# Kernel tuning notes

Measured on AMD Instinct MI355X. Metric: run time of the kernel, lower is better.

The kernel has to match this reference:

```python
import jax, jax.numpy as jnp
import numpy as np
import math

LMAX = 5
TAU_PRE = 16
TAU = 16
B = 256


def _cg_coeff(l1, l2, l, m1, m2, m):
    # Standard Clebsch-Gordan coefficient <l1 m1 l2 m2 | l m> (Racah formula).
    if m1 + m2 != m or l < abs(l1 - l2) or l > l1 + l2:
        return 0.0
    f = math.factorial
    pref = math.sqrt((2 * l + 1) * f(l + l1 - l2) * f(l - l1 + l2) * f(l1 + l2 - l) / f(l1 + l2 + l + 1))
    pref *= math.sqrt(f(l + m) * f(l - m) * f(l1 - m1) * f(l1 + m1) * f(l2 - m2) * f(l2 + m2))
    kmin = max(0, l2 - l - m1, l1 + m2 - l)
    kmax = min(l1 + l2 - l, l1 - m1, l2 + m2)
    s = 0.0
    for k in range(kmin, kmax + 1):
        s += (-1) ** k / (f(k) * f(l1 + l2 - l - k) * f(l1 - m1 - k) * f(l2 + m2 - k) * f(l - l2 + m1 + k) * f(l - l1 - m2 + k))
    return pref * s


def _build_cg(lmax):
    # Enumerate (l1, l2<=l1, l) triples exactly as UpdateFunction._calculate_number_of_cols / fCG do.
    triples, tensors = [], {}
    for l1 in range(lmax + 1):
        for l2 in range(l1 + 1):
            for l in range(abs(l1 - l2), min(l1 + l2 + 1, lmax + 1)):
                C = np.zeros((2 * l + 1, 2 * l1 + 1, 2 * l2 + 1), dtype=np.float32)
                for m in range(-l, l + 1):
                    for m1 in range(-l1, l1 + 1):
                        m2 = m - m1
                        if -l2 <= m2 <= l2:
                            C[m + l, m1 + l1, m2 + l2] = _cg_coeff(l1, l2, l, m1, m2, m)
                triples.append((l1, l2, l))
                tensors[(l1, l2, l)] = jnp.asarray(C)
    return triples, tensors


TRIPLES, CG = _build_cg(LMAX)
NUMCOLS = [sum(TAU_PRE * TAU_PRE for (_, _, l) in TRIPLES if l == L) for L in range(LMAX + 1)]


def _cg_transform(fs):
    # CG tensor product: for each (l1,l2,l) triple form complex channel-pair products
    # contracted with CG coefficients; concat fragments along the channel axis per l.
    frags = [[] for _ in range(LMAX + 1)]
    for (l1, l2, l) in TRIPLES:
        C = CG[(l1, l2, l)]                       # [2l+1, 2l1+1, 2l2+1]
        f1, f2 = fs[l1], fs[l2]                   # [B, t, 2l*+1, 2]
        f1r, f1i = f1[..., 0], f1[..., 1]
        f2r, f2i = f2[..., 0], f2[..., 1]
        rr = jnp.einsum('kmn,bim,bjn->bijk', C, f1r, f2r)
        ii = jnp.einsum('kmn,bim,bjn->bijk', C, f1i, f2i)
        ri = jnp.einsum('kmn,bim,bjn->bijk', C, f1r, f2i)
        ir = jnp.einsum('kmn,bim,bjn->bijk', C, f1i, f2r)
        frag = jnp.stack([rr - ii, ri + ir], axis=-1)          # [B, t1, t2, 2l+1, 2]
        bsz = f1.shape[0]
        frags[l].append(frag.reshape(bsz, -1, 2 * l + 1, 2))
    return [jnp.concatenate(fl, axis=1) for fl in frags]       # per l: [B, numcols[l], 2l+1, 2]


def _complex_mm(w, f):
    # Complex_bmm with w broadcast over the batch: w [tau, cols, 2], f [B, cols, 2l+1, 2].
    wr, wi = w[..., 0], w[..., 1]
    fr, fi = f[..., 0], f[..., 1]
    real = jnp.einsum('tc,bck->btk', wr, fr) - jnp.einsum('tc,bck->btk', wi, fi)
    imag = jnp.einsum('tc,bck->btk', wr, fi) + jnp.einsum('tc,bck->btk', wi, fr)
    return jnp.stack([real, imag], axis=-1)                    # [B, tau, 2l+1, 2]


def setup_inputs() -> dict:
    key = jax.random.key(0)
    inp = {}
    for l in range(LMAX + 1):
        inp['f%d' % l] = jax.random.normal(jax.random.fold_in(key, l), (B, TAU_PRE, 2 * l + 1, 2), dtype=jnp.float32)
        inp['w%d' % l] = 0.05 * jax.random.uniform(jax.random.fold_in(key, 100 + l), (TAU, NUMCOLS[l], 2), dtype=jnp.float32)
    return inp


def reference(f0, f1, f2, f3, f4, f5, w0, w1, w2, w3, w4, w5):
    fs = [f0, f1, f2, f3, f4, f5]
    ws = [w0, w1, w2, w3, w4, w5]
    new_fs = _cg_transform(fs)
    return tuple(_complex_mm(ws[l], new_fs[l]) for l in range(LMAX + 1))
```

## Files before the change

### kernel.cpp

```cpp
#include <hip/hip_runtime.h>
#include <hip/hip_fp16.h>
#include <utility>


using f32x4 = __attribute__((ext_vector_type(4))) float;
using f16x8 = __attribute__((ext_vector_type(8))) _Float16;

constexpr int OUTOFF_[6]  = {0, 8192, 32768, 73728, 131072, 204800};
constexpr int NUMCOLS_[6] = {1536, 2560, 3328, 3584, 3584, 3072};
constexpr int FOFFH_[6]   = {0, 16, 64, 144, 256, 400};
constexpr int WOFF_[6]    = {0, 49152, 131072, 237568, 352256, 466944};

constexpr int TRI_N[6] = {6, 10, 13, 14, 14, 12};
constexpr int TRI_L1[6][14] = {
    {0,1,2,3,4,5, 0,0,0,0,0,0,0,0},
    {1,1,2,2,3,3,4,4,5,5, 0,0,0,0},
    {1,2,2,2,3,3,3,4,4,4,5,5,5, 0},
    {2,2,3,3,3,3,4,4,4,4,5,5,5,5},
    {2,3,3,3,4,4,4,4,4,5,5,5,5,5},
    {3,3,4,4,4,4,5,5,5,5,5,5, 0,0}};
constexpr int TRI_L2[6][14] = {
    {0,1,2,3,4,5, 0,0,0,0,0,0,0,0},
    {0,1,1,2,2,3,3,4,4,5, 0,0,0,0},
    {1,0,1,2,1,2,3,2,3,4,3,4,5, 0},
    {1,2,0,1,2,3,1,2,3,4,2,3,4,5},
    {2,1,2,3,0,1,2,3,4,1,2,3,4,5},
    {2,3,1,2,3,4,0,1,2,3,4,5, 0,0}};

constexpr double cfact(int n) { double r = 1.0; for (int i = 2; i <= n; ++i) r *= (double)i; return r; }

constexpr double csqrt(double x) {
    if (x <= 0.0) return 0.0;
    double g = x < 1.0 ? 1.0 : x;
    for (int i = 0; i < 200; ++i) {
        double n = 0.5 * (g + x / g);
        if (n == g) break;
        g = n;
    }
    return g;
}

constexpr double cg_c(int l1, int l2, int l, int m1, int m2, int m) {
    double pref = (2.0 * l + 1.0) * cfact(l + l1 - l2) * cfact(l - l1 + l2) *
                  cfact(l1 + l2 - l) / cfact(l1 + l2 + l + 1);
    pref *= cfact(l + m) * cfact(l - m) * cfact(l1 - m1) * cfact(l1 + m1) *
            cfact(l2 - m2) * cfact(l2 + m2);
    pref = csqrt(pref);
    int kmin = 0;
    if (l2 - l - m1 > kmin) kmin = l2 - l - m1;
    if (l1 + m2 - l > kmin) kmin = l1 + m2 - l;
    int kmax = l1 + l2 - l;
    if (l1 - m1 < kmax) kmax = l1 - m1;
    if (l2 + m2 < kmax) kmax = l2 + m2;
    double s = 0.0;
    for (int k = kmin; k <= kmax; ++k) {
        double d = cfact(k) * cfact(l1 + l2 - l - k) * cfact(l1 - m1 - k) *
                   cfact(l2 + m2 - k) * cfact(l - l2 + m1 + k) * cfact(l - l1 - m2 + k);
        s += ((k & 1) ? -1.0 : 1.0) / d;
    }
    return pref * s;
}

template <int L1, int L2, int L>
struct CGTab {
    static constexpr int N1 = 2 * L1 + 1, N2 = 2 * L2 + 1;
    struct T { float v[N1 * N2]; };
    static constexpr T build() {
        T t{};
        for (int m1 = -L1; m1 <= L1; ++m1)
            for (int m2 = -L2; m2 <= L2; ++m2) {
                int m = m1 + m2;
                double v = 0.0;
                if (m >= -L && m <= L) v = cg_c(L1, L2, L, m1, m2, m);
                t.v[(m1 + L1) * N2 + (m2 + L2)] = (float)v;
            }
        return t;
    }
    static constexpr T TAB = build();
};

__global__ __launch_bounds__(256)
void wconv_kernel(const float* __restrict__ w0, const float* __restrict__ w1,
                  const float* __restrict__ w2, const float* __restrict__ w3,
                  const float* __restrict__ w4, const float* __restrict__ w5,
                  unsigned short* __restrict__ dst)
{
    const int l = blockIdx.y;
    const float* srcs[6] = {w0, w1, w2, w3, w4, w5};
    const float* src = srcs[l];
    const int cnt = 16 * NUMCOLS_[l] * 2;
    const int i4 = (blockIdx.x * 256 + threadIdx.x) * 4;
    if (i4 < cnt) {
        const float4 v = *(const float4*)(src + i4);
        __half hx = __float2half(v.x), hy = __float2half(v.y);
        __half hz = __float2half(v.z), hw = __float2half(v.w);
        ushort4 o;
        o.x = *(unsigned short*)&hx; o.y = *(unsigned short*)&hy;
        o.z = *(unsigned short*)&hz; o.w = *(unsigned short*)&hw;
        *(ushort4*)(dst + WOFF_[l] + i4) = o;
    }
}

template <int L, int L1, int L2>
__device__ __forceinline__ void do_phase1(const unsigned* __restrict__ sh_fh,
                                          char* __restrict__ frag, const int tid)
{
    constexpr int N1 = 2 * L1 + 1, N2 = 2 * L2 + 1, NK = 2 * L + 1, SH = L1 + L2 - L;
    const int i = tid >> 4, j = tid & 15;
    const unsigned* f1 = sh_fh + FOFFH_[L1] + i * N1;
    const unsigned* f2 = sh_fh + FOFFH_[L2] + j * N2;

    unsigned axx[N1], ayy[N1], bv[N2], bsn[N2];
#pragma unroll
    for (int m = 0; m < N1; ++m) {
        const unsigned a = f1[m];
        const unsigned lo = a & 0xffffu, hi = a >> 16;
        axx[m] = lo | (lo << 16);
        ayy[m] = hi | (hi << 16);
    }
#pragma unroll
    for (int n = 0; n < N2; ++n) {
        const unsigned b = f2[n];
        bv[n] = b;
        bsn[n] = ((b >> 16) | (b << 16)) ^ 0x8000u;
    }

    const int ij4 = tid * 4;
#pragma unroll
    for (int k = 0; k < NK; ++k) {
        const int kk = k + SH;
        __half2 acc = __float2half2_rn(0.0f);
#pragma unroll
        for (int m1 = 0; m1 < N1; ++m1) {
            const int m2 = kk - m1;
            if (m2 >= 0 && m2 < N2) {
                const float c = CGTab<L1, L2, L>::TAB.v[m1 * N2 + m2];
                if (c != 0.f) {
                    const __half2 p = __hfma2(*(const __half2*)&ayy[m1],
                                              *(const __half2*)&bsn[m2],
                                              __hmul2(*(const __half2*)&axx[m1],
                                                      *(const __half2*)&bv[m2]));
                    acc = __hfma2(__float2half2_rn(c), p, acc);
                }
            }
        }
        *(__half2*)(frag + ((k * 1024 + ij4) ^ ((k & 7) << 4))) = acc;
    }
}

template <int L>
__device__ __forceinline__ void do_mfma(const char* __restrict__ frag,
                                        const unsigned short* __restrict__ wh,
                                        const int cbase, const int wave,
                                        const int lane, f32x4& PR, f32x4& PI)
{
    constexpr int NK = 2 * L + 1;
    const int t = lane & 15, g = lane >> 4;
    int nc = lane & 15; if (nc > NK - 1) nc = NK - 1;
    const int C = NUMCOLS_[L];
#pragma unroll
    for (int ks = 0; ks < 4; ++ks) {
        const int c0 = wave * 64 + ks * 16 + 4 * g;
        uint4 wa = *(const uint4*)(wh + (size_t)(t * C + cbase + c0) * 2);
        uint4 a1, a2;
        a1.x = wa.x ^ 0x80000000u; a1.y = wa.y ^ 0x80000000u;
        a1.z = wa.z ^ 0x80000000u; a1.w = wa.w ^ 0x80000000u;
        a2.x = (wa.x >> 16) | (wa.x << 16); a2.y = (wa.y >> 16) | (wa.y << 16);
        a2.z = (wa.z >> 16) | (wa.z << 16); a2.w = (wa.w >> 16) | (wa.w << 16);
        const int byt = (nc * 1024 + c0 * 4) ^ ((nc & 7) << 4);
        const f16x8 B = *(const f16x8*)(frag + byt);
        PR = __builtin_amdgcn_mfma_f32_16x16x32_f16(*(const f16x8*)&a1, B, PR, 0, 0, 0);
        PI = __builtin_amdgcn_mfma_f32_16x16x32_f16(*(const f16x8*)&a2, B, PI, 0, 0, 0);
    }
}

template <int L, int IDX>
__device__ __forceinline__ void step(const unsigned* sh_fh, char* buf0, char* buf1,
                                     const unsigned short* wh, const int tid,
                                     const int wave, const int lane,
                                     f32x4& PR, f32x4& PI)
{
    constexpr int NT = TRI_N[L];
    if constexpr (IDX > 0)
        do_mfma<L>(((IDX - 1) & 1) ? buf1 : buf0, wh, (IDX - 1) * 256, wave, lane, PR, PI);
    if constexpr (IDX < NT)
        do_phase1<L, TRI_L1[L][IDX], TRI_L2[L][IDX]>(sh_fh, (IDX & 1) ? buf1 : buf0, tid);
    __syncthreads();
}

template <int L, int... Is>
__device__ __forceinline__ void run_steps(std::integer_sequence<int, Is...>,
    const unsigned* sh_fh, char* buf0, char* buf1, const unsigned short* wh,
    int tid, int wave, int lane, f32x4& PR, f32x4& PI)
{
    (step<L, Is>(sh_fh, buf0, buf1, wh, tid, wave, lane, PR, PI), ...);
}

template <int L>
__device__ void run_l(const float* const* fs, const unsigned short* __restrict__ wh,
                      float* __restrict__ out, unsigned* sh_fh, char* buf0, char* buf1)
{
    const int b = blockIdx.x, tid = threadIdx.x;
    const int wave = tid >> 6, lane = tid & 63;

#pragma unroll
    for (int l = 0; l < 6; ++l) {
        const int cnt = 16 * (2 * l + 1);
        const float2* s2 = (const float2*)(fs[l] + (size_t)b * 32 * (2 * l + 1));
        if (tid < cnt) {
            const float2 v = s2[tid];
            const __half2 h = __floats2half2_rn(v.x, v.y);
            sh_fh[FOFFH_[l] + tid] = *(const unsigned*)&h;
        }
    }
    __syncthreads();

    f32x4 PR = {0.f, 0.f, 0.f, 0.f}, PI = {0.f, 0.f, 0.f, 0.f};

    run_steps<L>(std::make_integer_sequence<int, TRI_N[L] + 1>{},
                 sh_fh, buf0, buf1, wh, tid, wave, lane, PR, PI);

    constexpr int NK = 2 * L + 1;
    float* pb = (float*)buf0;
    {
        const int kcol = lane & 15, g = lane >> 4;
#pragma unroll
        for (int r = 0; r < 4; ++r) {
            pb[(wave * 2 + 0) * 256 + (4 * g + r) * 16 + kcol] = PR[r];
            pb[(wave * 2 + 1) * 256 + (4 * g + r) * 16 + kcol] = PI[r];
        }
    }
    __syncthreads();

    if (tid < 16 * NK) {
        const int t = tid & 15, k = tid >> 4;
        float oR = 0.f, oI = 0.f;
#pragma unroll
        for (int w = 0; w < 4; ++w) {
            oR += pb[(w * 2 + 0) * 256 + t * 16 + k];
            oI += pb[(w * 2 + 1) * 256 + t * 16 + k];
        }
        float* op = out + OUTOFF_[L] + ((size_t)(b * 16 + t) * NK + k) * 2;
        op[0] = oR;
        op[1] = oI;
    }
}

__global__ __launch_bounds__(256, 5)
void update_kernel(const float* __restrict__ f0, const float* __restrict__ f1,
                   const float* __restrict__ f2, const float* __restrict__ f3,
                   const float* __restrict__ f4, const float* __restrict__ f5,
                   const unsigned short* __restrict__ wh,
                   float* __restrict__ out)
{
    __shared__ unsigned sh_fh[576];
    __shared__ __align__(16) char buf0[11264];
    __shared__ __align__(16) char buf1[11264];
    const float* fs[6] = {f0, f1, f2, f3, f4, f5};
    switch (blockIdx.y) {
        case 0: run_l<5>(fs, wh + WOFF_[5], out, sh_fh, buf0, buf1); break;
        case 1: run_l<4>(fs, wh + WOFF_[4], out, sh_fh, buf0, buf1); break;
        case 2: run_l<3>(fs, wh + WOFF_[3], out, sh_fh, buf0, buf1); break;
        case 3: run_l<2>(fs, wh + WOFF_[2], out, sh_fh, buf0, buf1); break;
        case 4: run_l<1>(fs, wh + WOFF_[1], out, sh_fh, buf0, buf1); break;
        default: run_l<0>(fs, wh + WOFF_[0], out, sh_fh, buf0, buf1); break;
    }
}

extern "C" void kernel_launch(void* const* d_in, const int* in_sizes, int n_in,
                              void* d_out, int out_size, void* d_ws, size_t ws_size,
                              hipStream_t stream)
{
    const float* f[6];
    const float* w[6];
    for (int l = 0; l < 6; ++l) {
        f[l] = (const float*)d_in[2 * l];
        w[l] = (const float*)d_in[2 * l + 1];
    }
    unsigned short* wh = (unsigned short*)d_ws;

    wconv_kernel<<<dim3(112, 6), dim3(256), 0, stream>>>(
        w[0], w[1], w[2], w[3], w[4], w[5], wh);

    update_kernel<<<dim3(256, 6), dim3(256), 0, stream>>>(
        f[0], f[1], f[2], f[3], f[4], f[5], wh, (float*)d_out);
}
```

Before: 121.8 us.

## Drop double-buffered fragment staging and per-step block barriers in CG kernel

Replaces the two ping-pong LDS fragment buffers with a single buffer. Each triple step now runs phase1 then the MFMA accumulation back to back, with no __syncthreads between steps, which relies on each wave writing exactly the fragment columns it later reads. A separate LDS array holds the reduction scratch, and launch bounds are raised to 6 blocks per CU to use the lower LDS footprint. This removes a block-wide barrier per triple and should raise occupancy. In exchange it loses the overlap between one step's MFMA and the next step's fragment build. If the column ownership is not actually wave-local, it introduces an LDS race.

After: 125.8 us. +3.3%, slower.

```diff
diff --git a/kernel.cpp b/kernel.cpp
--- a/kernel.cpp
+++ b/kernel.cpp
@@ -175,30 +175,26 @@
 }
 
 template <int L, int IDX>
-__device__ __forceinline__ void step(const unsigned* sh_fh, char* buf0, char* buf1,
+__device__ __forceinline__ void step(const unsigned* sh_fh, char* frag,
                                      const unsigned short* wh, const int tid,
                                      const int wave, const int lane,
                                      f32x4& PR, f32x4& PI)
 {
-    constexpr int NT = TRI_N[L];
-    if constexpr (IDX > 0)
-        do_mfma<L>(((IDX - 1) & 1) ? buf1 : buf0, wh, (IDX - 1) * 256, wave, lane, PR, PI);
-    if constexpr (IDX < NT)
-        do_phase1<L, TRI_L1[L][IDX], TRI_L2[L][IDX]>(sh_fh, (IDX & 1) ? buf1 : buf0, tid);
-    __syncthreads();
+    do_phase1<L, TRI_L1[L][IDX], TRI_L2[L][IDX]>(sh_fh, frag, tid);
+    do_mfma<L>(frag, wh, IDX * 256, wave, lane, PR, PI);
 }
 
 template <int L, int... Is>
 __device__ __forceinline__ void run_steps(std::integer_sequence<int, Is...>,
-    const unsigned* sh_fh, char* buf0, char* buf1, const unsigned short* wh,
+    const unsigned* sh_fh, char* frag, const unsigned short* wh,
     int tid, int wave, int lane, f32x4& PR, f32x4& PI)
 {
-    (step<L, Is>(sh_fh, buf0, buf1, wh, tid, wave, lane, PR, PI), ...);
+    (step<L, Is>(sh_fh, frag, wh, tid, wave, lane, PR, PI), ...);
 }
 
 template <int L>
 __device__ void run_l(const float* const* fs, const unsigned short* __restrict__ wh,
-                      float* __restrict__ out, unsigned* sh_fh, char* buf0, char* buf1)
+                      float* __restrict__ out, unsigned* sh_fh, char* frag, float* pb)
 {
     const int b = blockIdx.x, tid = threadIdx.x;
     const int wave = tid >> 6, lane = tid & 63;
@@ -217,11 +213,10 @@
 
     f32x4 PR = {0.f, 0.f, 0.f, 0.f}, PI = {0.f, 0.f, 0.f, 0.f};
 
-    run_steps<L>(std::make_integer_sequence<int, TRI_N[L] + 1>{},
-                 sh_fh, buf0, buf1, wh, tid, wave, lane, PR, PI);
+    run_steps<L>(std::make_integer_sequence<int, TRI_N[L]>{},
+                 sh_fh, frag, wh, tid, wave, lane, PR, PI);
 
     constexpr int NK = 2 * L + 1;
-    float* pb = (float*)buf0;
     {
         const int kcol = lane & 15, g = lane >> 4;
 #pragma unroll
@@ -246,7 +241,7 @@
     }
 }
 
-__global__ __launch_bounds__(256, 5)
+__global__ __launch_bounds__(256, 6)
 void update_kernel(const float* __restrict__ f0, const float* __restrict__ f1,
                    const float* __restrict__ f2, const float* __restrict__ f3,
                    const float* __restrict__ f4, const float* __restrict__ f5,
@@ -254,16 +249,16 @@
                    float* __restrict__ out)
 {
     __shared__ unsigned sh_fh[576];
-    __shared__ __align__(16) char buf0[11264];
-    __shared__ __align__(16) char buf1[11264];
+    __shared__ __align__(16) char frag[11264];
+    __shared__ __align__(16) float pb[2048];
     const float* fs[6] = {f0, f1, f2, f3, f4, f5};
     switch (blockIdx.y) {
-        case 0: run_l<5>(fs, wh + WOFF_[5], out, sh_fh, buf0, buf1); break;
-        case 1: run_l<4>(fs, wh + WOFF_[4], out, sh_fh, buf0, buf1); break;
-        case 2: run_l<3>(fs, wh + WOFF_[3], out, sh_fh, buf0, buf1); break;
-        case 3: run_l<2>(fs, wh + WOFF_[2], out, sh_fh, buf0, buf1); break;
-        case 4: run_l<1>(fs, wh + WOFF_[1], out, sh_fh, buf0, buf1); break;
-        default: run_l<0>(fs, wh + WOFF_[0], out, sh_fh, buf0, buf1); break;
+        case 0: run_l<5>(fs, wh + WOFF_[5], out, sh_fh, frag, pb); break;
+        case 1: run_l<4>(fs, wh + WOFF_[4], out, sh_fh, frag, pb); break;
+        case 2: run_l<3>(fs, wh + WOFF_[3], out, sh_fh, frag, pb); break;
+        case 3: run_l<2>(fs, wh + WOFF_[2], out, sh_fh, frag, pb); break;
+        case 4: run_l<1>(fs, wh + WOFF_[1], out, sh_fh, frag, pb); break;
+        default: run_l<0>(fs, wh + WOFF_[0], out, sh_fh, frag, pb); break;
     }
 }
 
```
